# Kernel tuning notes

Hardware: AMD Instinct MI355X
Metric: run time of the kernel (lower is better)

The kernel has to match this reference:

```python
import jax, jax.numpy as jnp
import numpy as np

QMAX = 127.0  # torch.iinfo(torch.int8).max


def setup_inputs() -> dict:
    key = jax.random.key(0)
    k1, k2 = jax.random.split(key)
    input_act = jax.random.normal(k1, (4, 2048, 4096), dtype=jnp.float32)
    # nn.Linear weight: [out_features, in_features], fp weights pre-quantization
    weight = jax.random.normal(k2, (4096, 4096), dtype=jnp.float32) * 0.02
    return {"input_act": input_act, "weight": weight}


def reference(input_act, weight):
    # --- weight_quant (per-channel over in_features) ---
    w_scale = jnp.max(jnp.abs(weight), axis=-1, keepdims=True) / QMAX      # [O, 1]
    w_q = jnp.round(weight / w_scale).astype(jnp.int8)                      # int8 weight

    # --- activation quant (per-token over last dim) ---
    a_scale = jnp.max(jnp.abs(input_act), axis=-1, keepdims=True) / QMAX    # [B, S, 1]
    x_q = jnp.round(input_act / a_scale).astype(jnp.int8)                   # int8 acts

    # --- int8 GEMM with int32 accumulation (torch._int_mm semantics) ---
    # [B, S, K] @ [K, O] -> [B, S, O]
    acc = jnp.matmul(x_q.astype(jnp.int32), w_q.T.astype(jnp.int32))        # exact int32

    # --- dequant: scale = input_act_scale * weight_scale.T, then cast to fp16 ---
    scale = a_scale * w_scale.T[None, :, :]                                 # [B, S, O]
    out = (acc.astype(jnp.float32) * scale).astype(jnp.float16)
    return out
```

## Files before the change

### kernel.cpp

```cpp
#include <hip/hip_runtime.h>
#include <hip/hip_fp16.h>
#include <cstdint>

typedef int v4i __attribute__((ext_vector_type(4)));

#define AS1C(p) ((const __attribute__((address_space(1))) void*)(p))
#define AS3(p)  ((__attribute__((address_space(3))) void*)(p))

__global__ __launch_bounds__(256) void quant_rows(const float* __restrict__ X,
                                                  int8_t* __restrict__ Q,
                                                  float* __restrict__ scales,
                                                  int K) {
    const int row = blockIdx.x;
    const float4* xv = (const float4*)(X + (size_t)row * K);
    const int nv = K >> 2;

    float m = 0.0f;
    for (int i = threadIdx.x; i < nv; i += 256) {
        float4 v = xv[i];
        m = fmaxf(m, fabsf(v.x));
        m = fmaxf(m, fabsf(v.y));
        m = fmaxf(m, fabsf(v.z));
        m = fmaxf(m, fabsf(v.w));
    }
    for (int off = 32; off > 0; off >>= 1)
        m = fmaxf(m, __shfl_xor(m, off, 64));

    __shared__ float wmax[4];
    __shared__ float s_sc;
    const int lane = threadIdx.x & 63;
    const int wv = threadIdx.x >> 6;
    if (lane == 0) wmax[wv] = m;
    __syncthreads();
    if (threadIdx.x == 0) {
        float mm = fmaxf(fmaxf(wmax[0], wmax[1]), fmaxf(wmax[2], wmax[3]));
        float sc = mm / 127.0f;
        scales[row] = sc;
        s_sc = sc;
    }
    __syncthreads();
    const float sc = s_sc;

    char4* qv = (char4*)(Q + (size_t)row * K);
    for (int i = threadIdx.x; i < nv; i += 256) {
        float4 v = xv[i];
        char4 q;
        q.x = (signed char)(int)rintf(v.x / sc);
        q.y = (signed char)(int)rintf(v.y / sc);
        q.z = (signed char)(int)rintf(v.z / sc);
        q.w = (signed char)(int)rintf(v.w / sc);
        qv[i] = q;
    }
}

__global__ __launch_bounds__(512, 2) void gemm_i8(const int8_t* __restrict__ Aq,
                                                  const int8_t* __restrict__ Bq,
                                                  const float* __restrict__ a_scale,
                                                  const float* __restrict__ w_scale,
                                                  float* __restrict__ out) {
    extern __shared__ __align__(16) int8_t smem[];

    const int K = 4096;
    const int bid = blockIdx.x;
    const int wg  = (bid & 7) * 64 + (bid >> 3);
    const int n0 = (wg & 15) * 256;
    const int m0 = (wg >> 4) * 256;

    const int tid  = threadIdx.x;
    const int lane = tid & 63;
    const int wid  = tid >> 6;
    const int wm   = wid >> 2;
    const int wn   = wid & 3;

    const int rsel  = lane & 15;
    const int kswz  = ((lane >> 4) << 4) ^ (((rsel >> 1) & 3) << 4);
    const int abase = (wm * 128 + rsel) * 64 + kswz;
    const int bbase = (wn * 64  + rsel) * 64 + kswz;

    const int strow = tid >> 2;
    const int stswz = ((strow >> 1) & 3) << 4;
    const int stcol = ((tid & 3) << 4) ^ stswz;
    const int8_t* gA = Aq + (size_t)(m0 + strow) * K + stcol;
    const int8_t* gB = Bq + (size_t)(n0 + strow) * K + stcol;
    const size_t rstep = (size_t)128 * K;
    const int ldsst = wid * 1024;

    v4i acc[8][4] = {};

#pragma unroll
    for (int kt = 0; kt < 3; ++kt) {
        int8_t* bA = smem + kt * 32768;
        int8_t* bB = bA + 16384;
        const int8_t* a = gA + kt * 64;
        const int8_t* b = gB + kt * 64;
        __builtin_amdgcn_global_load_lds(AS1C(a),         AS3(bA + ldsst),        16, 0, 0);
        __builtin_amdgcn_global_load_lds(AS1C(a + rstep), AS3(bA + 8192 + ldsst), 16, 0, 0);
        __builtin_amdgcn_global_load_lds(AS1C(b),         AS3(bB + ldsst),        16, 0, 0);
        __builtin_amdgcn_global_load_lds(AS1C(b + rstep), AS3(bB + 8192 + ldsst), 16, 0, 0);
    }
    asm volatile("s_waitcnt vmcnt(8)" ::: "memory");
    __builtin_amdgcn_s_barrier();

    for (int kt4 = 0; kt4 < 64; kt4 += 4) {
#pragma unroll
        for (int u = 0; u < 4; ++u) {
            const int kt = kt4 + u;
            const int8_t* bA = smem + u * 32768;
            const int8_t* bB = bA + 16384;
            int8_t* pA = smem + ((u + 3) & 3) * 32768;
            int8_t* pB = pA + 16384;
            const int ktp = (kt + 3 < 64) ? kt + 3 : 63;
            const int8_t* a = gA + (size_t)ktp * 64;
            const int8_t* b = gB + (size_t)ktp * 64;

            v4i aF[4], bF[4];
#pragma unroll
            for (int mt = 0; mt < 4; ++mt)
                aF[mt] = *(const v4i*)(bA + abase + mt * 1024);
#pragma unroll
            for (int nt = 0; nt < 4; ++nt)
                bF[nt] = *(const v4i*)(bB + bbase + nt * 1024);
            __builtin_amdgcn_global_load_lds(AS1C(a),         AS3(pA + ldsst),        16, 0, 0);
            __builtin_amdgcn_global_load_lds(AS1C(a + rstep), AS3(pA + 8192 + ldsst), 16, 0, 0);
            __builtin_amdgcn_s_barrier();
            __builtin_amdgcn_s_setprio(1);
#pragma unroll
            for (int mt = 0; mt < 4; ++mt)
#pragma unroll
                for (int nt = 0; nt < 4; ++nt)
                    acc[mt][nt] = __builtin_amdgcn_mfma_i32_16x16x64_i8(
                        aF[mt], bF[nt], acc[mt][nt], 0, 0, 0);
            __builtin_amdgcn_s_setprio(0);
            __builtin_amdgcn_s_barrier();

#pragma unroll
            for (int mt = 0; mt < 4; ++mt)
                aF[mt] = *(const v4i*)(bA + abase + (mt + 4) * 1024);
            __builtin_amdgcn_global_load_lds(AS1C(b),         AS3(pB + ldsst),        16, 0, 0);
            __builtin_amdgcn_global_load_lds(AS1C(b + rstep), AS3(pB + 8192 + ldsst), 16, 0, 0);
            __builtin_amdgcn_s_barrier();
            __builtin_amdgcn_s_setprio(1);
#pragma unroll
            for (int mt = 0; mt < 4; ++mt)
#pragma unroll
                for (int nt = 0; nt < 4; ++nt)
                    acc[mt + 4][nt] = __builtin_amdgcn_mfma_i32_16x16x64_i8(
                        aF[mt], bF[nt], acc[mt + 4][nt], 0, 0, 0);
            __builtin_amdgcn_s_setprio(0);
            asm volatile("s_waitcnt vmcnt(8)" ::: "memory");
            __builtin_amdgcn_s_barrier();
            __builtin_amdgcn_sched_barrier(0);
        }
    }

    const int r0  = (lane >> 4) << 2;
    const int col = lane & 15;
#pragma unroll
    for (int mt = 0; mt < 8; ++mt) {
        const int tbase = m0 + wm * 128 + mt * 16 + r0;
        float as[4];
#pragma unroll
        for (int r = 0; r < 4; ++r) as[r] = a_scale[tbase + r];
#pragma unroll
        for (int nt = 0; nt < 4; ++nt) {
            const int o = n0 + wn * 64 + nt * 16 + col;
            const float wsc = w_scale[o];
#pragma unroll
            for (int r = 0; r < 4; ++r) {
                float v = (float)acc[mt][nt][r] * as[r] * wsc;
                out[(size_t)(tbase + r) * 4096 + o] = __half2float(__float2half_rn(v));
            }
        }
    }
}

extern "C" void kernel_launch(void* const* d_in, const int* in_sizes, int n_in,
                              void* d_out, int out_size, void* d_ws, size_t ws_size,
                              hipStream_t stream) {
    const float* input_act = (const float*)d_in[0];
    const float* weight    = (const float*)d_in[1];
    float* out = (float*)d_out;

    const int K = 4096, O = 4096, T = 8192;

    int8_t* x_q = (int8_t*)d_ws;
    int8_t* w_q = x_q + (size_t)T * K;
    float* a_scale = (float*)(w_q + (size_t)O * K);
    float* w_scale = a_scale + T;

    static bool attr_done = false;
    if (!attr_done) {
        hipFuncSetAttribute(reinterpret_cast<const void*>(gemm_i8),
                            hipFuncAttributeMaxDynamicSharedMemorySize, 131072);
        attr_done = true;
    }

    quant_rows<<<T, 256, 0, stream>>>(input_act, x_q, a_scale, K);
    quant_rows<<<O, 256, 0, stream>>>(weight, w_q, w_scale, K);

    dim3 grid(512);
    gemm_i8<<<grid, 512, 131072, stream>>>(x_q, w_q, a_scale, w_scale, out);
}
```

Measured before the change: 196.8 us.

## Double-buffer MFMA fragments in registers and prefetch next K-step during compute

Restructures the int8 GEMM main loop so each K-step loads the next tile's A and B fragments from LDS into a second register set while MFMAs run on the current set. Barriers per K-step drop from three to one, and the LDS reads for the next step are interleaved with the MFMA issue. The cost is more VGPRs (two full fragment sets of 8 A and 4 B vectors) under the existing 512-thread, 2-block launch bounds, which could cause spills or lower occupancy. It also changes the vmcnt wait so that only the oldest stage must have landed.

```diff
diff --git a/kernel.cpp b/kernel.cpp
--- a/kernel.cpp
+++ b/kernel.cpp
@@ -75,7 +75,7 @@
     const int rsel  = lane & 15;
     const int kswz  = ((lane >> 4) << 4) ^ (((rsel >> 1) & 3) << 4);
     const int abase = (wm * 128 + rsel) * 64 + kswz;
-    const int bbase = (wn * 64  + rsel) * 64 + kswz;
+    const int bbase = 16384 + (wn * 64 + rsel) * 64 + kswz;
 
     const int strow = tid >> 2;
     const int stswz = ((strow >> 1) & 3) << 4;
@@ -86,71 +86,54 @@
     const int ldsst = wid * 1024;
 
     v4i acc[8][4] = {};
+    v4i aFa[8], aFb[8], bFa[4], bFb[4];
 
-#pragma unroll
-    for (int kt = 0; kt < 3; ++kt) {
-        int8_t* bA = smem + kt * 32768;
-        int8_t* bB = bA + 16384;
-        const int8_t* a = gA + kt * 64;
-        const int8_t* b = gB + kt * 64;
-        __builtin_amdgcn_global_load_lds(AS1C(a),         AS3(bA + ldsst),        16, 0, 0);
-        __builtin_amdgcn_global_load_lds(AS1C(a + rstep), AS3(bA + 8192 + ldsst), 16, 0, 0);
-        __builtin_amdgcn_global_load_lds(AS1C(b),         AS3(bB + ldsst),        16, 0, 0);
-        __builtin_amdgcn_global_load_lds(AS1C(b + rstep), AS3(bB + 8192 + ldsst), 16, 0, 0);
-    }
+#define STAGE(buf, kt) do {                                                          \
+    int8_t* _d = smem + (buf) * 32768;                                               \
+    const int8_t* _a = gA + (size_t)(kt) * 64;                                       \
+    const int8_t* _b = gB + (size_t)(kt) * 64;                                       \
+    __builtin_amdgcn_global_load_lds(AS1C(_a),         AS3(_d + ldsst),         16, 0, 0); \
+    __builtin_amdgcn_global_load_lds(AS1C(_a + rstep), AS3(_d + 8192  + ldsst), 16, 0, 0); \
+    __builtin_amdgcn_global_load_lds(AS1C(_b),         AS3(_d + 16384 + ldsst), 16, 0, 0); \
+    __builtin_amdgcn_global_load_lds(AS1C(_b + rstep), AS3(_d + 24576 + ldsst), 16, 0, 0); \
+  } while (0)
+
+#define KSTEP(u, CA, CB, NA, NB, kt4) do {                                           \
+    const int kt  = (kt4) + (u);                                                     \
+    const int8_t* bufN = smem + (((u) + 1) & 3) * 32768;                             \
+    const int ktp = (kt + 3 < 64) ? (kt + 3) : 63;                                   \
+    asm volatile("s_waitcnt vmcnt(4)" ::: "memory");                                 \
+    __builtin_amdgcn_s_barrier();                                                    \
+    _Pragma("unroll")                                                                \
+    for (int mt = 0; mt < 8; ++mt)                                                   \
+        NA[mt] = *(const v4i*)(bufN + abase + mt * 1024);                            \
+    STAGE(((u) + 3) & 3, ktp);                                                       \
+    __builtin_amdgcn_sched_barrier(0);                                               \
+    __builtin_amdgcn_s_setprio(1);                                                   \
+    _Pragma("unroll")                                                                \
+    for (int nt = 0; nt < 4; ++nt) {                                                 \
+        _Pragma("unroll")                                                            \
+        for (int mt = 0; mt < 8; ++mt)                                               \
+            acc[mt][nt] = __builtin_amdgcn_mfma_i32_16x16x64_i8(                     \
+                CA[mt], CB[nt], acc[mt][nt], 0, 0, 0);                               \
+        NB[nt] = *(const v4i*)(bufN + bbase + nt * 1024);                            \
+    }                                                                                \
+    __builtin_amdgcn_s_setprio(0);                                                   \
+  } while (0)
+
+    STAGE(0, 0); STAGE(1, 1); STAGE(2, 2);
     asm volatile("s_waitcnt vmcnt(8)" ::: "memory");
     __builtin_amdgcn_s_barrier();
+#pragma unroll
+    for (int mt = 0; mt < 8; ++mt) aFa[mt] = *(const v4i*)(smem + abase + mt * 1024);
+#pragma unroll
+    for (int nt = 0; nt < 4; ++nt) bFa[nt] = *(const v4i*)(smem + bbase + nt * 1024);
 
     for (int kt4 = 0; kt4 < 64; kt4 += 4) {
-#pragma unroll
-        for (int u = 0; u < 4; ++u) {
-            const int kt = kt4 + u;
-            const int8_t* bA = smem + u * 32768;
-            const int8_t* bB = bA + 16384;
-            int8_t* pA = smem + ((u + 3) & 3) * 32768;
-            int8_t* pB = pA + 16384;
-            const int ktp = (kt + 3 < 64) ? kt + 3 : 63;
-            const int8_t* a = gA + (size_t)ktp * 64;
-            const int8_t* b = gB + (size_t)ktp * 64;
-
-            v4i aF[4], bF[4];
-#pragma unroll
-            for (int mt = 0; mt < 4; ++mt)
-                aF[mt] = *(const v4i*)(bA + abase + mt * 1024);
-#pragma unroll
-            for (int nt = 0; nt < 4; ++nt)
-                bF[nt] = *(const v4i*)(bB + bbase + nt * 1024);
-            __builtin_amdgcn_global_load_lds(AS1C(a),         AS3(pA + ldsst),        16, 0, 0);
-            __builtin_amdgcn_global_load_lds(AS1C(a + rstep), AS3(pA + 8192 + ldsst), 16, 0, 0);
-            __builtin_amdgcn_s_barrier();
-            __builtin_amdgcn_s_setprio(1);
-#pragma unroll
-            for (int mt = 0; mt < 4; ++mt)
-#pragma unroll
-                for (int nt = 0; nt < 4; ++nt)
-                    acc[mt][nt] = __builtin_amdgcn_mfma_i32_16x16x64_i8(
-                        aF[mt], bF[nt], acc[mt][nt], 0, 0, 0);
-            __builtin_amdgcn_s_setprio(0);
-            __builtin_amdgcn_s_barrier();
-
-#pragma unroll
-            for (int mt = 0; mt < 4; ++mt)
-                aF[mt] = *(const v4i*)(bA + abase + (mt + 4) * 1024);
-            __builtin_amdgcn_global_load_lds(AS1C(b),         AS3(pB + ldsst),        16, 0, 0);
-            __builtin_amdgcn_global_load_lds(AS1C(b + rstep), AS3(pB + 8192 + ldsst), 16, 0, 0);
-            __builtin_amdgcn_s_barrier();
-            __builtin_amdgcn_s_setprio(1);
-#pragma unroll
-            for (int mt = 0; mt < 4; ++mt)
-#pragma unroll
-                for (int nt = 0; nt < 4; ++nt)
-                    acc[mt + 4][nt] = __builtin_amdgcn_mfma_i32_16x16x64_i8(
-                        aF[mt], bF[nt], acc[mt + 4][nt], 0, 0, 0);
-            __builtin_amdgcn_s_setprio(0);
-            asm volatile("s_waitcnt vmcnt(8)" ::: "memory");
-            __builtin_amdgcn_s_barrier();
-            __builtin_amdgcn_sched_barrier(0);
-        }
+        KSTEP(0, aFa, bFa, aFb, bFb, kt4);
+        KSTEP(1, aFb, bFb, aFa, bFa, kt4);
+        KSTEP(2, aFa, bFa, aFb, bFb, kt4);
+        KSTEP(3, aFb, bFb, aFa, bFa, kt4);
     }
 
     const int r0  = (lane >> 4) << 2;
@@ -172,6 +155,8 @@
             }
         }
     }
+#undef KSTEP
+#undef STAGE
 }
 
 extern "C" void kernel_launch(void* const* d_in, const int* in_sizes, int n_in,
```

Measured after the change: 195.7 us. No clear change (-0.6%).
